# Performance work log

Hardware: AMD Instinct MI355X
Metric: run time of the kernel (lower is better)

## Reference

```python
import jax, jax.numpy as jnp
import numpy as np

B, N, DIM, H, DH = 4, 16384, 256, 8, 32
INNER = H * DH
SCALE = DH ** -0.5


def setup_inputs() -> dict:
    key = jax.random.key(0)
    ks = jax.random.split(key, 15)
    g = lambda k, shape, s=0.02: jax.random.normal(k, shape, dtype=jnp.float32) * s
    return {
        "states": jax.random.normal(ks[0], (B, N, DIM), dtype=jnp.float32),
        "agent_qs": jax.random.normal(ks[1], (B, N, DIM), dtype=jnp.float32),
        "obs": jax.random.normal(ks[2], (B, N, DIM), dtype=jnp.float32),
        "Wq": g(ks[3], (DIM, INNER)), "bq": g(ks[4], (INNER,)),
        "Wk": g(ks[5], (DIM, INNER)), "bk": g(ks[6], (INNER,)),
        "Wv": g(ks[7], (DIM, INNER)), "bv": g(ks[8], (INNER,)),
        "wq_attn": g(ks[9], (DH,), 0.1),
        "wk_attn": g(ks[10], (DH,), 0.1),
        "Wr": g(ks[11], (DH, DH)), "br": g(ks[12], (DH,)),
        "Wout": g(ks[13], (INNER, DIM)), "bout": g(ks[14], (DIM,)),
    }


def _heads(t):
    # [b, n, h*d] -> [b, h, n, d]
    b, n, _ = t.shape
    return t.reshape(b, n, H, DH).transpose(0, 2, 1, 3)


def reference(states, agent_qs, obs, Wq, bq, Wk, bk, Wv, bv,
              wq_attn, wk_attn, Wr, br, Wout, bout):
    q = _heads(jnp.abs(states @ Wq + bq))   # b h n d
    k = _heads(agent_qs @ Wk + bk)          # b h n d
    v = _heads(obs @ Wv + bv)               # b h n d

    # additive attention pooling for global query
    q_attn = jax.nn.softmax(jnp.einsum('bhnd,d->bhn', q, wq_attn) * SCALE, axis=-1)
    global_q = jnp.einsum('bhn,bhnd->bhd', q_attn, q)  # b h d

    # gate keys with global query, pool against ORIGINAL k (k_aggr)
    k_gated = k * global_q[:, :, None, :]
    k_attn = jax.nn.softmax(jnp.einsum('bhnd,d->bhn', k_gated, wk_attn) * SCALE, axis=-1)
    global_k = jnp.einsum('bhn,bhnd->bhd', k_attn, k)  # b h d

    u = v * global_k[:, :, None, :]
    r = u @ Wr + br + q                      # b h n d
    r = r.transpose(0, 2, 1, 3).reshape(r.shape[0], r.shape[2], INNER)  # b n (h d)
    return r @ Wout + bout
```

## Files before the change

kernel.cpp:

```cpp
#include <hip/hip_runtime.h>
#include <hip/hip_bf16.h>

#define B_   4
#define N_   16384
#define T_   65536
static constexpr float SCALE_F = 0.17677669529663687f;

typedef __attribute__((ext_vector_type(8))) short bf16x8;
typedef __attribute__((ext_vector_type(4))) float f32x4;

#define BAR() __builtin_amdgcn_s_barrier()
#define WAIT(vm) asm volatile("s_waitcnt vmcnt(" #vm ") lgkmcnt(0)" ::: "memory")

template<int S> struct IC { static constexpr int v = S; };

static __device__ __forceinline__ unsigned pk2bf(float lo, float hi) {
    __hip_bfloat162 t = __float22bfloat162_rn(make_float2(lo, hi));
    union { __hip_bfloat162 h; unsigned u; } c; c.h = t; return c.u;
}
static __device__ __forceinline__ unsigned short f2bf(float f) {
    unsigned u = __float_as_uint(f);
    u += 0x7fffu + ((u >> 16) & 1u);
    return (unsigned short)(u >> 16);
}
static __device__ __forceinline__ void gl_lds16(const void* g, void* l) {
    __builtin_amdgcn_global_load_lds(
        (const __attribute__((address_space(1))) unsigned int*)g,
        (__attribute__((address_space(3))) unsigned int*)l, 16, 0, 0);
}

__global__ __launch_bounds__(256) void prep_all(
    const float* __restrict__ Wq, const float* __restrict__ Wk,
    const float* __restrict__ Wv, unsigned short* __restrict__ Wt,
    const float* __restrict__ Wr, const float* __restrict__ br,
    const float* __restrict__ Wout, const float* __restrict__ bout,
    float* __restrict__ S1t, float* __restrict__ cvec)
{
    const int blk = blockIdx.x;
    if (blk < 3) {
        const float* W = (blk == 0) ? Wq : (blk == 1) ? Wk : Wv;
        unsigned short* dst = Wt + (size_t)blk * 65536 + (size_t)threadIdx.x * 256;
        #pragma unroll 4
        for (int kb = 0; kb < 32; ++kb) {
            float v[8];
            #pragma unroll
            for (int e = 0; e < 8; ++e) v[e] = W[(kb*8 + e)*256 + threadIdx.x];
            uint4 w;
            w.x = pk2bf(v[0], v[1]); w.y = pk2bf(v[2], v[3]);
            w.z = pk2bf(v[4], v[5]); w.w = pk2bf(v[6], v[7]);
            *reinterpret_cast<uint4*>(dst + kb*8) = w;
        }
        return;
    }
    const int i = blk - 3, j = threadIdx.x;
    if (i < 256) {
        const int h = i >> 5, dd = i & 31;
        float s = 0.f;
        #pragma unroll 8
        for (int dp = 0; dp < 32; ++dp)
            s = fmaf(Wr[dd*32 + dp], Wout[(h*32 + dp)*256 + j], s);
        S1t[(size_t)j*256 + i] = s;
    } else {
        float cj = bout[j];
        for (int r = 0; r < 256; ++r) cj = fmaf(br[r & 31], Wout[r*256 + j], cj);
        cvec[j] = cj;
    }
}

__global__ __launch_bounds__(256, 2) void proj_mfma(
    const float* __restrict__ states, const float* __restrict__ agent_qs,
    const float* __restrict__ obs, const unsigned short* __restrict__ Wt,
    const float* __restrict__ bq, const float* __restrict__ bk,
    const float* __restrict__ bv,
    unsigned short* __restrict__ q_bf, unsigned short* __restrict__ k_bf,
    unsigned short* __restrict__ v_bf)
{
    __shared__ __align__(16) float As[4][64*32];

    const int tid = threadIdx.x;
    const int z  = blockIdx.y;
    const int t0 = blockIdx.x * 64;

    const float* X = (z == 0) ? states : (z == 1) ? agent_qs : obs;
    const unsigned short* Bt = Wt + (size_t)z * 65536;
    const float* bias = (z == 0) ? bq : (z == 1) ? bk : bv;
    unsigned short* Y = (z == 0) ? q_bf : (z == 1) ? k_bf : v_bf;
    const bool doabs = (z == 0);

    const int wid = tid >> 6, lane = tid & 63;
    const int l15 = lane & 15, g = lane >> 4;
    const int wc = wid;

    const unsigned short* bbase[4];
    #pragma unroll
    for (int ni = 0; ni < 4; ++ni) {
        int np = ni*16 + l15;
        int c = (np & 32) | ((np & 12) << 1) | ((np & 16) >> 2) | (np & 3);
        bbase[ni] = Bt + (size_t)(wc*64 + c) * 256 + g*8;
    }

    bf16x8 breg[4][4];
    auto loadBhalf = [&](int half) {
        #pragma unroll
        for (int ni = 0; ni < 4; ++ni)
            #pragma unroll
            for (int sl = 0; sl < 4; ++sl)
                breg[ni][sl] = *reinterpret_cast<const bf16x8*>(
                    bbase[ni] + (half*4 + sl)*32);
    };

    const int srow_lane = lane >> 3;
    const int schunk = (lane & 7) ^ (lane >> 3);
    auto stageA = [&](int buf, int step) {
        const int k0 = step * 32;
        #pragma unroll
        for (int i = 0; i < 2; ++i) {
            int r = (wid*2 + i)*8 + srow_lane;
            gl_lds16(X + (size_t)(t0 + r)*256 + k0 + schunk*4,
                     &As[buf][(wid*2 + i)*256]);
        }
    };

    f32x4 acc[4][4];
    #pragma unroll
    for (int mi = 0; mi < 4; ++mi)
        #pragma unroll
        for (int ni = 0; ni < 4; ++ni) acc[mi][ni] = (f32x4){0.f,0.f,0.f,0.f};

    auto body = [&](auto sc) {
        constexpr int s = decltype(sc)::v;
        constexpr int buf = s & 3;
        constexpr int sl  = s & 3;
        bf16x8 a[4];
        #pragma unroll
        for (int mi = 0; mi < 4; ++mi) {
            int m = mi*16 + l15;
            int x = m & 7;
            f32x4 lo = *reinterpret_cast<const f32x4*>(&As[buf][m*32 + ((2*g)  ^x)*4]);
            f32x4 hi = *reinterpret_cast<const f32x4*>(&As[buf][m*32 + ((2*g+1)^x)*4]);
            union { unsigned u[4]; bf16x8 v; } cc;
            cc.u[0] = pk2bf(lo[0], lo[1]);
            cc.u[1] = pk2bf(lo[2], lo[3]);
            cc.u[2] = pk2bf(hi[0], hi[1]);
            cc.u[3] = pk2bf(hi[2], hi[3]);
            a[mi] = cc.v;
        }
        if constexpr (s + 3 < 8) stageA((s + 3) & 3, s + 3);
        #pragma unroll
        for (int mi = 0; mi < 4; ++mi)
            #pragma unroll
            for (int ni = 0; ni < 4; ++ni)
                acc[mi][ni] = __builtin_amdgcn_mfma_f32_16x16x32_bf16(
                    breg[ni][sl], a[mi], acc[mi][ni], 0, 0, 0);
    };

    loadBhalf(0);
    stageA(0, 0); stageA(1, 1); stageA(2, 2);

    WAIT(4); BAR(); body(IC<0>{});
    WAIT(4); BAR(); body(IC<1>{});
    WAIT(4); BAR(); body(IC<2>{});
    WAIT(4); BAR(); body(IC<3>{});
    WAIT(0); BAR(); loadBhalf(1); body(IC<4>{});
    body(IC<5>{});
    body(IC<6>{});
    WAIT(0); BAR(); body(IC<7>{});

    #pragma unroll
    for (int s = 0; s < 2; ++s) {
        int colb = wc*64 + s*32 + g*8;
        float4 b0 = *reinterpret_cast<const float4*>(bias + colb);
        float4 b1 = *reinterpret_cast<const float4*>(bias + colb + 4);
        #pragma unroll
        for (int mi = 0; mi < 4; ++mi) {
            int m = t0 + mi*16 + l15;
            float y0 = acc[mi][2*s  ][0] + b0.x;
            float y1 = acc[mi][2*s  ][1] + b0.y;
            float y2 = acc[mi][2*s  ][2] + b0.z;
            float y3 = acc[mi][2*s  ][3] + b0.w;
            float y4 = acc[mi][2*s+1][0] + b1.x;
            float y5 = acc[mi][2*s+1][1] + b1.y;
            float y6 = acc[mi][2*s+1][2] + b1.z;
            float y7 = acc[mi][2*s+1][3] + b1.w;
            if (doabs) {
                y0 = fabsf(y0); y1 = fabsf(y1); y2 = fabsf(y2); y3 = fabsf(y3);
                y4 = fabsf(y4); y5 = fabsf(y5); y6 = fabsf(y6); y7 = fabsf(y7);
            }
            uint4 pk;
            pk.x = pk2bf(y0, y1); pk.y = pk2bf(y2, y3);
            pk.z = pk2bf(y4, y5); pk.w = pk2bf(y6, y7);
            *reinterpret_cast<uint4*>(Y + (size_t)m*256 + colb) = pk;
        }
    }
}

__global__ __launch_bounds__(512) void pool_partial(
    const unsigned short* __restrict__ data,
    const float* __restrict__ wqa, const float* __restrict__ wka,
    const float* __restrict__ part_in, float* __restrict__ part_out, int mode)
{
    const int bh = blockIdx.x, ch = blockIdx.y;
    const int b = bh >> 3, h = bh & 7;
    const int tid = threadIdx.x;

    __shared__ float coef[32];
    __shared__ float s_red[8];
    __shared__ float a_red[8][32];

    if (tid < 32) {
        float cc;
        if (mode == 0) cc = wqa[tid];
        else {
            float num = 0.f, den = 0.f;
            #pragma unroll
            for (int c = 0; c < 8; ++c) {
                num += part_in[(size_t)(bh*8 + c)*40 + tid];
                den += part_in[(size_t)(bh*8 + c)*40 + 32];
            }
            cc = (num / den) * wka[tid];
        }
        coef[tid] = cc * SCALE_F;
    }
    __syncthreads();
    float cf[32];
    #pragma unroll
    for (int d = 0; d < 32; ++d) cf[d] = coef[d];

    float s = 0.f;
    float acc[32];
    #pragma unroll
    for (int d = 0; d < 32; ++d) acc[d] = 0.f;

    const unsigned short* base = data + (size_t)b * N_ * 256 + h * 32;
    for (int n = ch*2048 + tid; n < (ch + 1)*2048; n += 512) {
        const uint4* p = reinterpret_cast<const uint4*>(base + (size_t)n * 256);
        float qv[32];
        #pragma unroll
        for (int gg = 0; gg < 4; ++gg) {
            uint4 r = p[gg];
            unsigned w0 = r.x, w1 = r.y, w2 = r.z, w3 = r.w;
            qv[gg*8+0] = __uint_as_float(w0 << 16);
            qv[gg*8+1] = __uint_as_float(w0 & 0xffff0000u);
            qv[gg*8+2] = __uint_as_float(w1 << 16);
            qv[gg*8+3] = __uint_as_float(w1 & 0xffff0000u);
            qv[gg*8+4] = __uint_as_float(w2 << 16);
            qv[gg*8+5] = __uint_as_float(w2 & 0xffff0000u);
            qv[gg*8+6] = __uint_as_float(w3 << 16);
            qv[gg*8+7] = __uint_as_float(w3 & 0xffff0000u);
        }
        float l = 0.f;
        #pragma unroll
        for (int d = 0; d < 32; ++d) l = fmaf(qv[d], cf[d], l);
        float e = expf(l);
        s += e;
        #pragma unroll
        for (int d = 0; d < 32; ++d) acc[d] = fmaf(e, qv[d], acc[d]);
    }

    #pragma unroll
    for (int off = 1; off < 64; off <<= 1) {
        s += __shfl_xor(s, off);
        #pragma unroll
        for (int d = 0; d < 32; ++d) acc[d] += __shfl_xor(acc[d], off);
    }
    const int wave = tid >> 6, lane = tid & 63;
    if (lane == 0) {
        s_red[wave] = s;
        #pragma unroll
        for (int d = 0; d < 32; ++d) a_red[wave][d] = acc[d];
    }
    __syncthreads();
    if (tid < 32) {
        float num = 0.f, den = 0.f;
        #pragma unroll
        for (int w2 = 0; w2 < 8; ++w2) { num += a_red[w2][tid]; den += s_red[w2]; }
        part_out[(size_t)(bh*8 + ch)*40 + tid] = num;
        if (tid == 0) part_out[(size_t)(bh*8 + ch)*40 + 32] = den;
    }
}

__global__ __launch_bounds__(256) void build_wcat_t(
    const float* __restrict__ part_k, const float* __restrict__ S1t,
    const float* __restrict__ Wout, unsigned short* __restrict__ Wcat_t)
{
    const int b = blockIdx.x, n = blockIdx.y, k = threadIdx.x;
    const int h = k >> 5, d = k & 31;
    float num = 0.f, den = 0.f;
    #pragma unroll
    for (int c = 0; c < 8; ++c) {
        num += part_k[(size_t)((b*8 + h)*8 + c)*40 + d];
        den += part_k[(size_t)((b*8 + h)*8 + c)*40 + 32];
    }
    const float gkv = num / den;
    unsigned short* dst = Wcat_t + (size_t)(b*256 + n) * 512;
    dst[k]       = f2bf(gkv * S1t[(size_t)n*256 + k]);
    dst[k + 256] = f2bf(Wout[(size_t)k*256 + n]);
}

__global__ __launch_bounds__(256, 2) void out_mfma(
    const unsigned short* __restrict__ v_bf, const unsigned short* __restrict__ q_bf,
    const unsigned short* __restrict__ Wcat_t, const float* __restrict__ cvec,
    float* __restrict__ out)
{
    __shared__ __align__(16) unsigned short As[4][64*32];

    const int tid = threadIdx.x;
    const int t0 = blockIdx.x * 64;
    const int b  = t0 >> 14;
    const unsigned short* Wb = Wcat_t + (size_t)b * 256 * 512;

    const int wid = tid >> 6, lane = tid & 63;
    const int l15 = lane & 15, g = lane >> 4, wc = wid;

    const unsigned short* bbase[4];
    #pragma unroll
    for (int ni = 0; ni < 4; ++ni)
        bbase[ni] = Wb + (size_t)(wc*64 + ni*16 + l15) * 512 + g*8;

    bf16x8 breg[4][8];
    auto loadBhalf = [&](int half) {
        #pragma unroll
        for (int ni = 0; ni < 4; ++ni)
            #pragma unroll
            for (int sl = 0; sl < 8; ++sl)
                breg[ni][sl] = *reinterpret_cast<const bf16x8*>(
                    bbase[ni] + (half*8 + sl)*32);
    };

    const int sr = wid*16 + (lane >> 2);
    const int stc = (lane & 3) ^ (sr & 3) ^ ((sr >> 2) & 3);
    auto stageA = [&](int buf, int step) {
        const int k0 = step * 32;
        const unsigned short* src = (k0 < 256) ? v_bf : q_bf;
        int ks = k0 & 255;
        gl_lds16(src + (size_t)(t0 + sr)*256 + ks + stc*8, &As[buf][wid*512]);
    };

    f32x4 acc[4][4];
    #pragma unroll
    for (int mi = 0; mi < 4; ++mi)
        #pragma unroll
        for (int ni = 0; ni < 4; ++ni) acc[mi][ni] = (f32x4){0.f,0.f,0.f,0.f};

    auto body = [&](auto sc) {
        constexpr int s = decltype(sc)::v;
        constexpr int buf = s & 3;
        constexpr int sl  = s & 7;
        bf16x8 a[4];
        #pragma unroll
        for (int mi = 0; mi < 4; ++mi) {
            int m = mi*16 + l15;
            int cc = g ^ (m & 3) ^ ((m >> 2) & 3);
            a[mi] = *reinterpret_cast<const bf16x8*>(&As[buf][m*32 + cc*8]);
        }
        if constexpr (s + 3 < 16) stageA((s + 3) & 3, s + 3);
        #pragma unroll
        for (int mi = 0; mi < 4; ++mi)
            #pragma unroll
            for (int ni = 0; ni < 4; ++ni)
                acc[mi][ni] = __builtin_amdgcn_mfma_f32_16x16x32_bf16(
                    breg[ni][sl], a[mi], acc[mi][ni], 0, 0, 0);
    };

    loadBhalf(0);
    stageA(0, 0); stageA(1, 1); stageA(2, 2);

    WAIT(2); BAR(); body(IC<0>{});
    WAIT(2); BAR(); body(IC<1>{});
    WAIT(2); BAR(); body(IC<2>{});
    WAIT(2); BAR(); body(IC<3>{});
    WAIT(2); BAR(); body(IC<4>{});
    WAIT(2); BAR(); body(IC<5>{});
    WAIT(2); BAR(); body(IC<6>{});
    WAIT(2); BAR(); body(IC<7>{});
    WAIT(0); BAR(); loadBhalf(1); body(IC<8>{});
    WAIT(2); BAR(); body(IC<9>{});
    WAIT(2); BAR(); body(IC<10>{});
    WAIT(2); BAR(); body(IC<11>{});
    WAIT(2); BAR(); body(IC<12>{});
    WAIT(2); BAR(); body(IC<13>{});
    WAIT(1); BAR(); body(IC<14>{});
    WAIT(0); BAR(); body(IC<15>{});

    #pragma unroll
    for (int ni = 0; ni < 4; ++ni) {
        int colb = wc*64 + ni*16 + g*4;
        float4 cv = *reinterpret_cast<const float4*>(cvec + colb);
        #pragma unroll
        for (int mi = 0; mi < 4; ++mi) {
            int m = t0 + mi*16 + l15;
            float4 o;
            o.x = acc[mi][ni][0] + cv.x;
            o.y = acc[mi][ni][1] + cv.y;
            o.z = acc[mi][ni][2] + cv.z;
            o.w = acc[mi][ni][3] + cv.w;
            *reinterpret_cast<float4*>(out + (size_t)m*256 + colb) = o;
        }
    }
}

extern "C" void kernel_launch(void* const* d_in, const int* in_sizes, int n_in,
                              void* d_out, int out_size, void* d_ws, size_t ws_size,
                              hipStream_t stream)
{
    const float* states   = (const float*)d_in[0];
    const float* agent_qs = (const float*)d_in[1];
    const float* obs      = (const float*)d_in[2];
    const float* Wq   = (const float*)d_in[3];
    const float* bq   = (const float*)d_in[4];
    const float* Wk   = (const float*)d_in[5];
    const float* bk   = (const float*)d_in[6];
    const float* Wv   = (const float*)d_in[7];
    const float* bv   = (const float*)d_in[8];
    const float* wq_attn = (const float*)d_in[9];
    const float* wk_attn = (const float*)d_in[10];
    const float* Wr   = (const float*)d_in[11];
    const float* br   = (const float*)d_in[12];
    const float* Wout = (const float*)d_in[13];
    const float* bout = (const float*)d_in[14];
    float* out = (float*)d_out;

    char* w = (char*)d_ws;
    unsigned short* q_bf = (unsigned short*)w; w += (size_t)T_ * 256 * 2;
    unsigned short* k_bf = (unsigned short*)w; w += (size_t)T_ * 256 * 2;
    unsigned short* v_bf = (unsigned short*)w; w += (size_t)T_ * 256 * 2;
    unsigned short* Wt_bf   = (unsigned short*)w; w += (size_t)3 * 65536 * 2;
    unsigned short* Wcat_t  = (unsigned short*)w; w += (size_t)4 * 256 * 512 * 2;
    float* part_q = (float*)w; w += (size_t)256 * 40 * sizeof(float);
    float* part_k = (float*)w; w += (size_t)256 * 40 * sizeof(float);
    float* S1t  = (float*)w; w += (size_t)256 * 256 * sizeof(float);
    float* cvec = (float*)w; w += 256 * sizeof(float);

    prep_all<<<dim3(260), 256, 0, stream>>>(Wq, Wk, Wv, Wt_bf,
                                            Wr, br, Wout, bout, S1t, cvec);
    proj_mfma<<<dim3(1024, 3), 256, 0, stream>>>(
        states, agent_qs, obs, Wt_bf, bq, bk, bv, q_bf, k_bf, v_bf);
    pool_partial<<<dim3(32, 8), 512, 0, stream>>>(q_bf, wq_attn, wk_attn,
                                                  part_q, part_q, 0);
    pool_partial<<<dim3(32, 8), 512, 0, stream>>>(k_bf, wq_attn, wk_attn,
                                                  part_q, part_k, 1);
    build_wcat_t<<<dim3(4, 256), 256, 0, stream>>>(part_k, S1t, Wout, Wcat_t);
    out_mfma<<<dim3(1024), 256, 0, stream>>>(v_bf, q_bf, Wcat_t, cvec, out);
}
```

Measured before the change: 202.1 us.

## Fuse q softmax pooling into projection epilogue and drop q pool pass

Computes the q attention logits, exponentials and the weighted sums directly in the proj_mfma epilogue from the fp32 values. These are reduced across lanes and accumulated with atomics into a zeroed global buffer, which removes the separate pool_partial pass that re-read q_bf. The k pooling kernel is split into twice as many chunks. Barriers plus s_setprio are added around the MFMA loops, and proj_mfma's occupancy hint is raised to 3. The softmax runs without max subtraction, so it relies on the logits being small, and the atomic order is nondeterministic.

```diff
diff --git a/kernel.cpp b/kernel.cpp
--- a/kernel.cpp
+++ b/kernel.cpp
@@ -11,6 +11,7 @@
 
 #define BAR() __builtin_amdgcn_s_barrier()
 #define WAIT(vm) asm volatile("s_waitcnt vmcnt(" #vm ") lgkmcnt(0)" ::: "memory")
+#define PRIO(p) __builtin_amdgcn_s_setprio(p)
 
 template<int S> struct IC { static constexpr int v = S; };
 
@@ -34,7 +35,8 @@
     const float* __restrict__ Wv, unsigned short* __restrict__ Wt,
     const float* __restrict__ Wr, const float* __restrict__ br,
     const float* __restrict__ Wout, const float* __restrict__ bout,
-    float* __restrict__ S1t, float* __restrict__ cvec)
+    float* __restrict__ S1t, float* __restrict__ cvec,
+    float* __restrict__ gq_buf)
 {
     const int blk = blockIdx.x;
     if (blk < 3) {
@@ -60,20 +62,27 @@
         for (int dp = 0; dp < 32; ++dp)
             s = fmaf(Wr[dd*32 + dp], Wout[(h*32 + dp)*256 + j], s);
         S1t[(size_t)j*256 + i] = s;
-    } else {
+    } else if (i == 256) {
         float cj = bout[j];
         for (int r = 0; r < 256; ++r) cj = fmaf(br[r & 31], Wout[r*256 + j], cj);
         cvec[j] = cj;
-    }
-}
-
-__global__ __launch_bounds__(256, 2) void proj_mfma(
+    } else {
+        #pragma unroll
+        for (int r = 0; r < 5; ++r) {
+            int idx = r*256 + j;
+            if (idx < 1056) gq_buf[idx] = 0.f;
+        }
+    }
+}
+
+__global__ __launch_bounds__(256, 3) void proj_mfma(
     const float* __restrict__ states, const float* __restrict__ agent_qs,
     const float* __restrict__ obs, const unsigned short* __restrict__ Wt,
     const float* __restrict__ bq, const float* __restrict__ bk,
-    const float* __restrict__ bv,
+    const float* __restrict__ bv, const float* __restrict__ wqa,
     unsigned short* __restrict__ q_bf, unsigned short* __restrict__ k_bf,
-    unsigned short* __restrict__ v_bf)
+    unsigned short* __restrict__ v_bf,
+    float* __restrict__ gq_num, float* __restrict__ gq_den)
 {
     __shared__ __align__(16) float As[4][64*32];
 
@@ -146,12 +155,15 @@
             a[mi] = cc.v;
         }
         if constexpr (s + 3 < 8) stageA((s + 3) & 3, s + 3);
+        BAR();
+        PRIO(1);
         #pragma unroll
         for (int mi = 0; mi < 4; ++mi)
             #pragma unroll
             for (int ni = 0; ni < 4; ++ni)
                 acc[mi][ni] = __builtin_amdgcn_mfma_f32_16x16x32_bf16(
                     breg[ni][sl], a[mi], acc[mi][ni], 0, 0, 0);
+        PRIO(0);
     };
 
     loadBhalf(0);
@@ -166,6 +178,18 @@
     body(IC<6>{});
     WAIT(0); BAR(); body(IC<7>{});
 
+    float wq8[8];
+    if (doabs) {
+        #pragma unroll
+        for (int j = 0; j < 8; ++j) wq8[j] = wqa[g*8 + j];
+    }
+    float numj[2][8];
+    float dena[2] = {0.f, 0.f};
+    #pragma unroll
+    for (int s = 0; s < 2; ++s)
+        #pragma unroll
+        for (int j = 0; j < 8; ++j) numj[s][j] = 0.f;
+
     #pragma unroll
     for (int s = 0; s < 2; ++s) {
         int colb = wc*64 + s*32 + g*8;
@@ -174,30 +198,66 @@
         #pragma unroll
         for (int mi = 0; mi < 4; ++mi) {
             int m = t0 + mi*16 + l15;
-            float y0 = acc[mi][2*s  ][0] + b0.x;
-            float y1 = acc[mi][2*s  ][1] + b0.y;
-            float y2 = acc[mi][2*s  ][2] + b0.z;
-            float y3 = acc[mi][2*s  ][3] + b0.w;
-            float y4 = acc[mi][2*s+1][0] + b1.x;
-            float y5 = acc[mi][2*s+1][1] + b1.y;
-            float y6 = acc[mi][2*s+1][2] + b1.z;
-            float y7 = acc[mi][2*s+1][3] + b1.w;
+            float y[8];
+            y[0] = acc[mi][2*s  ][0] + b0.x;
+            y[1] = acc[mi][2*s  ][1] + b0.y;
+            y[2] = acc[mi][2*s  ][2] + b0.z;
+            y[3] = acc[mi][2*s  ][3] + b0.w;
+            y[4] = acc[mi][2*s+1][0] + b1.x;
+            y[5] = acc[mi][2*s+1][1] + b1.y;
+            y[6] = acc[mi][2*s+1][2] + b1.z;
+            y[7] = acc[mi][2*s+1][3] + b1.w;
             if (doabs) {
-                y0 = fabsf(y0); y1 = fabsf(y1); y2 = fabsf(y2); y3 = fabsf(y3);
-                y4 = fabsf(y4); y5 = fabsf(y5); y6 = fabsf(y6); y7 = fabsf(y7);
+                #pragma unroll
+                for (int j = 0; j < 8; ++j) y[j] = fabsf(y[j]);
             }
             uint4 pk;
-            pk.x = pk2bf(y0, y1); pk.y = pk2bf(y2, y3);
-            pk.z = pk2bf(y4, y5); pk.w = pk2bf(y6, y7);
+            pk.x = pk2bf(y[0], y[1]); pk.y = pk2bf(y[2], y[3]);
+            pk.z = pk2bf(y[4], y[5]); pk.w = pk2bf(y[6], y[7]);
             *reinterpret_cast<uint4*>(Y + (size_t)m*256 + colb) = pk;
-        }
-    }
-}
-
-__global__ __launch_bounds__(512) void pool_partial(
+            if (doabs) {
+                float lp = 0.f;
+                #pragma unroll
+                for (int j = 0; j < 8; ++j) lp = fmaf(y[j], wq8[j], lp);
+                lp += __shfl_xor(lp, 16);
+                lp += __shfl_xor(lp, 32);
+                float e = expf(SCALE_F * lp);
+                dena[s] += e;
+                #pragma unroll
+                for (int j = 0; j < 8; ++j) numj[s][j] = fmaf(e, y[j], numj[s][j]);
+            }
+        }
+    }
+    if (doabs) {
+        #pragma unroll
+        for (int off = 1; off < 16; off <<= 1) {
+            #pragma unroll
+            for (int s = 0; s < 2; ++s) {
+                dena[s] += __shfl_xor(dena[s], off);
+                #pragma unroll
+                for (int j = 0; j < 8; ++j)
+                    numj[s][j] += __shfl_xor(numj[s][j], off);
+            }
+        }
+        if (l15 == 0) {
+            int b = t0 >> 14;
+            #pragma unroll
+            for (int s = 0; s < 2; ++s) {
+                int h = wc*2 + s;
+                #pragma unroll
+                for (int j = 0; j < 8; ++j)
+                    atomicAdd(&gq_num[(b*8 + h)*32 + g*8 + j], numj[s][j]);
+                if (g == 0) atomicAdd(&gq_den[b*8 + h], dena[s]);
+            }
+        }
+    }
+}
+
+__global__ __launch_bounds__(512) void pool_k(
     const unsigned short* __restrict__ data,
-    const float* __restrict__ wqa, const float* __restrict__ wka,
-    const float* __restrict__ part_in, float* __restrict__ part_out, int mode)
+    const float* __restrict__ wka,
+    const float* __restrict__ gq_num, const float* __restrict__ gq_den,
+    float* __restrict__ part_out)
 {
     const int bh = blockIdx.x, ch = blockIdx.y;
     const int b = bh >> 3, h = bh & 7;
@@ -208,18 +268,8 @@
     __shared__ float a_red[8][32];
 
     if (tid < 32) {
-        float cc;
-        if (mode == 0) cc = wqa[tid];
-        else {
-            float num = 0.f, den = 0.f;
-            #pragma unroll
-            for (int c = 0; c < 8; ++c) {
-                num += part_in[(size_t)(bh*8 + c)*40 + tid];
-                den += part_in[(size_t)(bh*8 + c)*40 + 32];
-            }
-            cc = (num / den) * wka[tid];
-        }
-        coef[tid] = cc * SCALE_F;
+        float gq = gq_num[bh*32 + tid] / gq_den[bh];
+        coef[tid] = gq * wka[tid] * SCALE_F;
     }
     __syncthreads();
     float cf[32];
@@ -232,7 +282,7 @@
     for (int d = 0; d < 32; ++d) acc[d] = 0.f;
 
     const unsigned short* base = data + (size_t)b * N_ * 256 + h * 32;
-    for (int n = ch*2048 + tid; n < (ch + 1)*2048; n += 512) {
+    for (int n = ch*1024 + tid; n < (ch + 1)*1024; n += 512) {
         const uint4* p = reinterpret_cast<const uint4*>(base + (size_t)n * 256);
         float qv[32];
         #pragma unroll
@@ -274,8 +324,8 @@
         float num = 0.f, den = 0.f;
         #pragma unroll
         for (int w2 = 0; w2 < 8; ++w2) { num += a_red[w2][tid]; den += s_red[w2]; }
-        part_out[(size_t)(bh*8 + ch)*40 + tid] = num;
-        if (tid == 0) part_out[(size_t)(bh*8 + ch)*40 + 32] = den;
+        part_out[(size_t)(bh*16 + ch)*40 + tid] = num;
+        if (tid == 0) part_out[(size_t)(bh*16 + ch)*40 + 32] = den;
     }
 }
 
@@ -287,9 +337,9 @@
     const int h = k >> 5, d = k & 31;
     float num = 0.f, den = 0.f;
     #pragma unroll
-    for (int c = 0; c < 8; ++c) {
-        num += part_k[(size_t)((b*8 + h)*8 + c)*40 + d];
-        den += part_k[(size_t)((b*8 + h)*8 + c)*40 + 32];
+    for (int c = 0; c < 16; ++c) {
+        num += part_k[(size_t)((b*8 + h)*16 + c)*40 + d];
+        den += part_k[(size_t)((b*8 + h)*16 + c)*40 + 32];
     }
     const float gkv = num / den;
     unsigned short* dst = Wcat_t + (size_t)(b*256 + n) * 512;
@@ -354,12 +404,15 @@
             a[mi] = *reinterpret_cast<const bf16x8*>(&As[buf][m*32 + cc*8]);
         }
         if constexpr (s + 3 < 16) stageA((s + 3) & 3, s + 3);
+        BAR();
+        PRIO(1);
         #pragma unroll
         for (int mi = 0; mi < 4; ++mi)
             #pragma unroll
             for (int ni = 0; ni < 4; ++ni)
                 acc[mi][ni] = __builtin_amdgcn_mfma_f32_16x16x32_bf16(
                     breg[ni][sl], a[mi], acc[mi][ni], 0, 0, 0);
+        PRIO(0);
     };
 
     loadBhalf(0);
@@ -426,19 +479,20 @@
     unsigned short* v_bf = (unsigned short*)w; w += (size_t)T_ * 256 * 2;
     unsigned short* Wt_bf   = (unsigned short*)w; w += (size_t)3 * 65536 * 2;
     unsigned short* Wcat_t  = (unsigned short*)w; w += (size_t)4 * 256 * 512 * 2;
-    float* part_q = (float*)w; w += (size_t)256 * 40 * sizeof(float);
-    float* part_k = (float*)w; w += (size_t)256 * 40 * sizeof(float);
+    float* gq_num = (float*)w; w += 1024 * sizeof(float);
+    float* gq_den = (float*)w; w += 32 * sizeof(float);
+    float* part_k = (float*)w; w += (size_t)32 * 16 * 40 * sizeof(float);
     float* S1t  = (float*)w; w += (size_t)256 * 256 * sizeof(float);
     float* cvec = (float*)w; w += 256 * sizeof(float);
 
-    prep_all<<<dim3(260), 256, 0, stream>>>(Wq, Wk, Wv, Wt_bf,
-                                            Wr, br, Wout, bout, S1t, cvec);
+    prep_all<<<dim3(261), 256, 0, stream>>>(Wq, Wk, Wv, Wt_bf,
+                                            Wr, br, Wout, bout, S1t, cvec,
+                                            gq_num);
     proj_mfma<<<dim3(1024, 3), 256, 0, stream>>>(
-        states, agent_qs, obs, Wt_bf, bq, bk, bv, q_bf, k_bf, v_bf);
-    pool_partial<<<dim3(32, 8), 512, 0, stream>>>(q_bf, wq_attn, wk_attn,
-                                                  part_q, part_q, 0);
-    pool_partial<<<dim3(32, 8), 512, 0, stream>>>(k_bf, wq_attn, wk_attn,
-                                                  part_q, part_k, 1);
+        states, agent_qs, obs, Wt_bf, bq, bk, bv, wq_attn,
+        q_bf, k_bf, v_bf, gq_num, gq_den);
+    pool_k<<<dim3(32, 16), 512, 0, stream>>>(k_bf, wk_attn, gq_num, gq_den,
+                                             part_k);
     build_wcat_t<<<dim3(4, 256), 256, 0, stream>>>(part_k, S1t, Wout, Wcat_t);
     out_mfma<<<dim3(1024), 256, 0, stream>>>(v_bf, q_bf, Wcat_t, cvec, out);
 }
```

New measurement: 280.2 us. +38.7%, slower.
